# Performance work log

Hardware: AMD Instinct MI355X
Metric: run time of the kernel (lower is better)

Reference implementation:

```python
import jax, jax.numpy as jnp
import numpy as np

# module hyperparams (from init_kwargs)
C, O, G, E, W, KS = 64, 64, 16, 128, 7, 2
AH, AS = 2, 2              # activate_height, activate_stride
D = C // G                 # kernel depth per group = 4
N = O // G                 # filters per group = 4
EPS = 1e-5                 # BatchNorm eps
LEAKY = 0.01               # LeakyReLU negative slope
B, T = 2, 512


def setup_inputs() -> dict:
    key = jax.random.key(0)
    k1, k2 = jax.random.split(key)
    x = jax.random.normal(k1, (B, C, E, T), dtype=jnp.float32)
    weight = jax.random.normal(k2, (O, D, E, W), dtype=jnp.float32) * 0.05
    gamma = jnp.ones((O,), jnp.float32)
    beta = jnp.zeros((O,), jnp.float32)
    return {"x": x, "weight": weight, "gamma": gamma, "beta": beta}


def reference(x, weight, gamma, beta):
    b, c, f, T_in = x.shape
    pad = W // 2
    xp = jnp.pad(x, ((0, 0), (0, 0), (0, 0), (pad, pad)))
    t = (T_in + 2 * pad - W) // KS + 1
    # unfold: window index grid [t, W]
    idx = KS * jnp.arange(t)[:, None] + jnp.arange(W)[None, :]
    xu = xp[..., idx]                        # [b, c, f, t, W]
    xu = xu.reshape(b, G, D, f, t, W)        # channel = (g d), group-major
    wg = weight.reshape(G, N, D, f, W)       # out = (g n)
    # broadcast elementwise mul -> [b, g, n, d, f, t, w]
    y = xu[:, :, None] * wg[None, :, :, :, :, None, :]
    y = y.reshape(b, O, D, f, t, W)          # (g n) -> o
    # BatchNorm3d over channel O, training-mode batch stats (biased var)
    mean = y.mean(axis=(0, 2, 3, 4, 5), keepdims=True)
    var = y.var(axis=(0, 2, 3, 4, 5), keepdims=True)
    y = (y - mean) * jax.lax.rsqrt(var + EPS)
    bshape = (1, O, 1, 1, 1, 1)
    y = y * gamma.reshape(bshape) + beta.reshape(bshape)
    ys = y.sum(axis=(2, 5))                  # [b, o, f, t]
    yp = jax.lax.reduce_window(ys, jnp.float32(0), jax.lax.add,
                               (1, 1, AH, 1), (1, 1, AS, 1), 'VALID')  # [b,o,fo,t]
    return jnp.where(yp >= 0, yp, LEAKY * yp)
```

## Files before the change

kernel.cpp:

```cpp
#include <hip/hip_runtime.h>

constexpr int Cc = 64, Oc = 64, Gc = 16, Ec = 128, Wc = 7;
constexpr int Dc = 4, Nc = 4, Bc = 2, Tc = 512, TTc = 256, FOc = 64;
constexpr float EPSf = 1e-5f, LEAKYf = 0.01f;
constexpr float Minv = 1.0f / 1835008.0f;


__device__ __forceinline__ int FL4(int c) { return (c & 3) * 33 + (c >> 2); }

__global__ __launch_bounds__(256) void fused_k(const float* __restrict__ x,
                                               const float* __restrict__ wgt,
                                               float* __restrict__ raw,
                                               float* __restrict__ partials) {
  int bid = blockIdx.x;
  int fo2 = bid & 31;
  int g   = (bid >> 5) & 15;
  int b   = bid >> 9;
  int t   = threadIdx.x;

  __shared__ float xs[16 * 528];
  __shared__ float wsm[512];
  __shared__ float QS[16][2];
  __shared__ float QL[16][7];

  float4* xs4 = (float4*)xs;

#pragma unroll
  for (int k = 0; k < 8; ++k) {
    int idx = t + 256 * k;
    int lr = idx >> 7, jj = idx & 127;
    int fo_l = lr >> 3, dd = (lr >> 1) & 3, f2 = lr & 1;
    const float4* src = (const float4*)(
        x + ((size_t)((b * Cc + g * Dc + dd) * Ec + 4 * fo2 + 2 * fo_l + f2)) * Tc);
    float4 v = src[jj];
    xs4[lr * 132 + FL4(jj + 1)] = v;
  }
  if (t < 32) {
    int lr = t >> 1;
    int c = (t & 1) ? 129 : 0;
    xs4[lr * 132 + FL4(c)] = make_float4(0.f, 0.f, 0.f, 0.f);
  }
  if (t < 128) {
#pragma unroll
    for (int i = 0; i < 4; ++i) {
      int s = t * 4 + i;
      int w = s & 7, n = (s >> 3) & 3, lr8 = (s >> 5) & 7, fo_l = s >> 8;
      int o = g * Nc + n, dd = lr8 >> 1, f = 4 * fo2 + 2 * fo_l + (lr8 & 1);
      wsm[s] = (w < 7) ? wgt[((size_t)((o * Dc + dd) * Ec + f)) * Wc + w] : 0.f;
    }
  }
  __syncthreads();

  {
    int row = t >> 4, sub = t & 15;
    float se2 = 0.f, so2 = 0.f;
#pragma unroll
    for (int k = 0; k < 8; ++k) {
      int c = 1 + sub + 16 * k;
      float4 v = xs4[row * 132 + FL4(c)];
      se2 += v.x * v.x + v.z * v.z;
      so2 += v.y * v.y + v.w * v.w;
    }
#pragma unroll
    for (int off = 1; off < 16; off <<= 1) {
      se2 += __shfl_xor(se2, off);
      so2 += __shfl_xor(so2, off);
    }
    if (sub == 0) { QS[row][0] = se2; QS[row][1] = so2; }
  }

  int wv = t >> 6, j = t & 63;
  int fo_l = wv >> 1, n0 = (wv & 1) * 2;
  int fo = fo2 * 2 + fo_l;
  float acc0[4] = {0.f, 0.f, 0.f, 0.f}, acc1[4] = {0.f, 0.f, 0.f, 0.f};
#pragma unroll
  for (int lr8 = 0; lr8 < 8; ++lr8) {
    const float4* rb = xs4 + (fo_l * 8 + lr8) * 132;
    float4 X0 = rb[FL4(2 * j)];
    float4 X1 = rb[FL4(2 * j + 1)];
    float4 X2 = rb[FL4(2 * j + 2)];
    float4 X3 = rb[FL4(2 * j + 3)];
    float xq[16] = {X0.x, X0.y, X0.z, X0.w, X1.x, X1.y, X1.z, X1.w,
                    X2.x, X2.y, X2.z, X2.w, X3.x, X3.y, X3.z, X3.w};
    const float4* wb = (const float4*)&wsm[((fo_l * 8 + lr8) * 4 + n0) * 8];
    float4 Wa0 = wb[0], Wa1 = wb[1], Wb0 = wb[2], Wb1 = wb[3];
    float wA[7] = {Wa0.x, Wa0.y, Wa0.z, Wa0.w, Wa1.x, Wa1.y, Wa1.z};
    float wB[7] = {Wb0.x, Wb0.y, Wb0.z, Wb0.w, Wb1.x, Wb1.y, Wb1.z};
#pragma unroll
    for (int w = 0; w < 7; ++w) {
#pragma unroll
      for (int s = 0; s < 4; ++s) {
        float xv = xq[2 * s + w + 1];
        acc0[s] += xv * wA[w];
        acc1[s] += xv * wB[w];
      }
    }
  }
  {
    int o0 = g * Nc + n0;
    float4 r0 = make_float4(acc0[0], acc0[1], acc0[2], acc0[3]);
    float4 r1 = make_float4(acc1[0], acc1[1], acc1[2], acc1[3]);
    *(float4*)(raw + ((size_t)((b * Oc + o0) * FOc + fo)) * TTc + 4 * j) = r0;
    *(float4*)(raw + ((size_t)((b * Oc + o0 + 1) * FOc + fo)) * TTc + 4 * j) = r1;
  }
  {
    float ms0 = acc0[0] + acc0[1] + acc0[2] + acc0[3];
    float ms1 = acc1[0] + acc1[1] + acc1[2] + acc1[3];
#pragma unroll
    for (int off = 1; off < 64; off <<= 1) {
      ms0 += __shfl_xor(ms0, off);
      ms1 += __shfl_xor(ms1, off);
    }
    if (j == 0) {
      float* p = &partials[((size_t)((b * Gc + g) * FOc + fo)) * 8];
      p[n0] = ms0;
      p[n0 + 1] = ms1;
    }
  }
  __syncthreads();

  if (t < 16) {
    int row = t;
    const float* rowf = &xs[row * 528];
    float e509 = rowf[129], e510 = rowf[130], e511 = rowf[131];
    float e0 = rowf[132], e1 = rowf[133];
    float se2 = QS[row][0], so2 = QS[row][1];
    QL[row][0] = so2 - e509 * e509 - e511 * e511;
    QL[row][1] = se2 - e510 * e510;
    QL[row][2] = so2 - e511 * e511;
    QL[row][3] = se2;
    QL[row][4] = so2;
    QL[row][5] = se2 - e0 * e0;
    QL[row][6] = so2 - e1 * e1;
  }
  __syncthreads();
  if (t < 8) {
    int fl = t >> 2, n = t & 3;
    float vp = 0.f;
#pragma unroll
    for (int lr8 = 0; lr8 < 8; ++lr8) {
#pragma unroll
      for (int w = 0; w < 7; ++w) {
        float wt = wsm[((fl * 8 + lr8) * 4 + n) * 8 + w];
        vp += QL[fl * 8 + lr8][w] * wt * wt;
      }
    }
    partials[((size_t)((b * Gc + g) * FOc + fo2 * 2 + fl)) * 8 + 4 + n] = vp;
  }
}

__global__ __launch_bounds__(256) void finish_k(const float* __restrict__ raw,
                                                const float* __restrict__ partials,
                                                const float* __restrict__ gamma,
                                                const float* __restrict__ beta,
                                                float* __restrict__ out) {
  int bid = blockIdx.x;
  int seg = bid & 15;
  int o   = (bid >> 4) & 63;
  int b   = bid >> 10;
  int tid = threadIdx.x;
  int g = o >> 2, n = o & 3;

  __shared__ float red[2][2];
  __shared__ float sAC[2];

  float mp = 0.f, vp = 0.f;
  if (tid < 128) {
    int b2 = tid >> 6, fo = tid & 63;
    const float* p = &partials[(size_t)(((b2 << 4) | g) << 6 | fo) * 8];
    mp = p[n];
    vp = p[4 + n];
  }
#pragma unroll
  for (int off = 1; off < 64; off <<= 1) {
    mp += __shfl_xor(mp, off);
    vp += __shfl_xor(vp, off);
  }
  int lane = tid & 63, wv = tid >> 6;
  if (lane == 0 && wv < 2) { red[wv][0] = mp; red[wv][1] = vp; }
  __syncthreads();
  if (tid == 0) {
    float mean = (red[0][0] + red[1][0]) * Minv;
    float e2   = (red[0][1] + red[1][1]) * Minv;
    float var  = e2 - mean * mean;
    float a    = gamma[o] * rsqrtf(var + EPSf);
    sAC[0] = a;
    sAC[1] = 56.0f * (beta[o] - a * mean);
  }
  __syncthreads();

  float a = sAC[0], c = sAC[1];
  size_t base = ((size_t)(b * Oc + o)) * (FOc * TTc) + seg * 1024 + tid * 4;
  float4 v = *(const float4*)(raw + base);
  float4 res;
  float r0 = a * v.x + c; res.x = (r0 >= 0.f) ? r0 : LEAKYf * r0;
  float r1 = a * v.y + c; res.y = (r1 >= 0.f) ? r1 : LEAKYf * r1;
  float r2 = a * v.z + c; res.z = (r2 >= 0.f) ? r2 : LEAKYf * r2;
  float r3 = a * v.w + c; res.w = (r3 >= 0.f) ? r3 : LEAKYf * r3;
  *(float4*)(out + base) = res;
}

extern "C" void kernel_launch(void* const* d_in, const int* in_sizes, int n_in,
                              void* d_out, int out_size, void* d_ws, size_t ws_size,
                              hipStream_t stream) {
  (void)in_sizes; (void)n_in; (void)out_size; (void)ws_size;
  const float* x     = (const float*)d_in[0];
  const float* w     = (const float*)d_in[1];
  const float* gamma = (const float*)d_in[2];
  const float* beta  = (const float*)d_in[3];
  float* raw      = (float*)d_ws;
  float* partials = raw + (size_t)Bc * Oc * FOc * TTc;
  fused_k<<<dim3(Bc * Gc * 32), dim3(256), 0, stream>>>(x, w, raw, partials);
  finish_k<<<dim3(Bc * Oc * 16), dim3(256), 0, stream>>>(raw, partials, gamma,
                                                         beta, (float*)d_out);
}
```

Before: 91.89 us.

## Fuse conv and batchnorm finish via grid-wide atomic barrier, keeping results in registers

Result: slower. 135.3 us (+47.2%).

```diff
diff --git a/kernel.cpp b/kernel.cpp
--- a/kernel.cpp
+++ b/kernel.cpp
@@ -3,201 +3,226 @@
 constexpr int Cc = 64, Oc = 64, Gc = 16, Ec = 128, Wc = 7;
 constexpr int Dc = 4, Nc = 4, Bc = 2, Tc = 512, TTc = 256, FOc = 64;
 constexpr float EPSf = 1e-5f, LEAKYf = 0.01f;
+constexpr unsigned NBLK = 512;
 constexpr float Minv = 1.0f / 1835008.0f;
 
 
 __device__ __forceinline__ int FL4(int c) { return (c & 3) * 33 + (c >> 2); }
 
-__global__ __launch_bounds__(256) void fused_k(const float* __restrict__ x,
-                                               const float* __restrict__ wgt,
-                                               float* __restrict__ raw,
-                                               float* __restrict__ partials) {
+__global__ __launch_bounds__(256, 2) void coop_k(
+    const float* __restrict__ x, const float* __restrict__ wgt,
+    float* __restrict__ partials, unsigned* __restrict__ cnt,
+    const float* __restrict__ gamma, const float* __restrict__ beta,
+    float* __restrict__ out) {
   int bid = blockIdx.x;
-  int fo2 = bid & 31;
-  int g   = (bid >> 5) & 15;
-  int b   = bid >> 9;
-  int t   = threadIdx.x;
+  int fp = bid & 15;
+  int g  = (bid >> 4) & 15;
+  int b  = bid >> 8;
+  int t  = threadIdx.x;
 
   __shared__ float xs[16 * 528];
   __shared__ float wsm[512];
   __shared__ float QS[16][2];
   __shared__ float QL[16][7];
+  __shared__ float SR[2][8];
+  __shared__ float sA[4], sC[4];
 
   float4* xs4 = (float4*)xs;
-
-#pragma unroll
-  for (int k = 0; k < 8; ++k) {
-    int idx = t + 256 * k;
-    int lr = idx >> 7, jj = idx & 127;
-    int fo_l = lr >> 3, dd = (lr >> 1) & 3, f2 = lr & 1;
-    const float4* src = (const float4*)(
-        x + ((size_t)((b * Cc + g * Dc + dd) * Ec + 4 * fo2 + 2 * fo_l + f2)) * Tc);
-    float4 v = src[jj];
-    xs4[lr * 132 + FL4(jj + 1)] = v;
-  }
-  if (t < 32) {
-    int lr = t >> 1;
-    int c = (t & 1) ? 129 : 0;
-    xs4[lr * 132 + FL4(c)] = make_float4(0.f, 0.f, 0.f, 0.f);
-  }
-  if (t < 128) {
-#pragma unroll
-    for (int i = 0; i < 4; ++i) {
-      int s = t * 4 + i;
-      int w = s & 7, n = (s >> 3) & 3, lr8 = (s >> 5) & 7, fo_l = s >> 8;
-      int o = g * Nc + n, dd = lr8 >> 1, f = 4 * fo2 + 2 * fo_l + (lr8 & 1);
-      wsm[s] = (w < 7) ? wgt[((size_t)((o * Dc + dd) * Ec + f)) * Wc + w] : 0.f;
-    }
-  }
-  __syncthreads();
-
-  {
-    int row = t >> 4, sub = t & 15;
-    float se2 = 0.f, so2 = 0.f;
-#pragma unroll
-    for (int k = 0; k < 8; ++k) {
-      int c = 1 + sub + 16 * k;
-      float4 v = xs4[row * 132 + FL4(c)];
-      se2 += v.x * v.x + v.z * v.z;
-      so2 += v.y * v.y + v.w * v.w;
-    }
-#pragma unroll
-    for (int off = 1; off < 16; off <<= 1) {
-      se2 += __shfl_xor(se2, off);
-      so2 += __shfl_xor(so2, off);
-    }
-    if (sub == 0) { QS[row][0] = se2; QS[row][1] = so2; }
-  }
 
   int wv = t >> 6, j = t & 63;
   int fo_l = wv >> 1, n0 = (wv & 1) * 2;
-  int fo = fo2 * 2 + fo_l;
-  float acc0[4] = {0.f, 0.f, 0.f, 0.f}, acc1[4] = {0.f, 0.f, 0.f, 0.f};
-#pragma unroll
-  for (int lr8 = 0; lr8 < 8; ++lr8) {
-    const float4* rb = xs4 + (fo_l * 8 + lr8) * 132;
-    float4 X0 = rb[FL4(2 * j)];
-    float4 X1 = rb[FL4(2 * j + 1)];
-    float4 X2 = rb[FL4(2 * j + 2)];
-    float4 X3 = rb[FL4(2 * j + 3)];
-    float xq[16] = {X0.x, X0.y, X0.z, X0.w, X1.x, X1.y, X1.z, X1.w,
-                    X2.x, X2.y, X2.z, X2.w, X3.x, X3.y, X3.z, X3.w};
-    const float4* wb = (const float4*)&wsm[((fo_l * 8 + lr8) * 4 + n0) * 8];
-    float4 Wa0 = wb[0], Wa1 = wb[1], Wb0 = wb[2], Wb1 = wb[3];
-    float wA[7] = {Wa0.x, Wa0.y, Wa0.z, Wa0.w, Wa1.x, Wa1.y, Wa1.z};
-    float wB[7] = {Wb0.x, Wb0.y, Wb0.z, Wb0.w, Wb1.x, Wb1.y, Wb1.z};
-#pragma unroll
-    for (int w = 0; w < 7; ++w) {
-#pragma unroll
-      for (int s = 0; s < 4; ++s) {
-        float xv = xq[2 * s + w + 1];
-        acc0[s] += xv * wA[w];
-        acc1[s] += xv * wB[w];
-      }
-    }
-  }
+
+  float accT[2][2][4];
+
+#pragma unroll
+  for (int k = 0; k < 2; ++k) {
+    int fo2 = fp * 2 + k;
+
+#pragma unroll
+    for (int kk = 0; kk < 8; ++kk) {
+      int idx = t + 256 * kk;
+      int lr = idx >> 7, jj = idx & 127;
+      int flS = lr >> 3, dd = (lr >> 1) & 3, f2 = lr & 1;
+      const float4* src = (const float4*)(
+          x + ((size_t)((b * Cc + g * Dc + dd) * Ec + 4 * fo2 + 2 * flS + f2)) * Tc);
+      float4 v = src[jj];
+      xs4[lr * 132 + FL4(jj + 1)] = v;
+    }
+    if (t < 32) {
+      int lr = t >> 1;
+      int c = (t & 1) ? 129 : 0;
+      xs4[lr * 132 + FL4(c)] = make_float4(0.f, 0.f, 0.f, 0.f);
+    }
+    if (t < 128) {
+#pragma unroll
+      for (int i = 0; i < 4; ++i) {
+        int s = t * 4 + i;
+        int w = s & 7, n = (s >> 3) & 3, lr8 = (s >> 5) & 7, flS = s >> 8;
+        int o = g * Nc + n, dd = lr8 >> 1, f = 4 * fo2 + 2 * flS + (lr8 & 1);
+        wsm[s] = (w < 7) ? wgt[((size_t)((o * Dc + dd) * Ec + f)) * Wc + w] : 0.f;
+      }
+    }
+    __syncthreads();
+
+    {
+      int row = t >> 4, sub = t & 15;
+      float se2 = 0.f, so2 = 0.f;
+#pragma unroll
+      for (int kk = 0; kk < 8; ++kk) {
+        int c = 1 + sub + 16 * kk;
+        float4 v = xs4[row * 132 + FL4(c)];
+        se2 += v.x * v.x + v.z * v.z;
+        so2 += v.y * v.y + v.w * v.w;
+      }
+#pragma unroll
+      for (int off = 1; off < 16; off <<= 1) {
+        se2 += __shfl_xor(se2, off);
+        so2 += __shfl_xor(so2, off);
+      }
+      if (sub == 0) { QS[row][0] = se2; QS[row][1] = so2; }
+    }
+
+    float acc0[4] = {0.f, 0.f, 0.f, 0.f}, acc1[4] = {0.f, 0.f, 0.f, 0.f};
+#pragma unroll
+    for (int lr8 = 0; lr8 < 8; ++lr8) {
+      const float4* rb = xs4 + (fo_l * 8 + lr8) * 132;
+      float4 X0 = rb[FL4(2 * j)];
+      float4 X1 = rb[FL4(2 * j + 1)];
+      float4 X2 = rb[FL4(2 * j + 2)];
+      float4 X3 = rb[FL4(2 * j + 3)];
+      float xq[16] = {X0.x, X0.y, X0.z, X0.w, X1.x, X1.y, X1.z, X1.w,
+                      X2.x, X2.y, X2.z, X2.w, X3.x, X3.y, X3.z, X3.w};
+      const float4* wb = (const float4*)&wsm[((fo_l * 8 + lr8) * 4 + n0) * 8];
+      float4 Wa0 = wb[0], Wa1 = wb[1], Wb0 = wb[2], Wb1 = wb[3];
+      float wA[7] = {Wa0.x, Wa0.y, Wa0.z, Wa0.w, Wa1.x, Wa1.y, Wa1.z};
+      float wB[7] = {Wb0.x, Wb0.y, Wb0.z, Wb0.w, Wb1.x, Wb1.y, Wb1.z};
+#pragma unroll
+      for (int w = 0; w < 7; ++w) {
+#pragma unroll
+        for (int s = 0; s < 4; ++s) {
+          float xv = xq[2 * s + w + 1];
+          acc0[s] += xv * wA[w];
+          acc1[s] += xv * wB[w];
+        }
+      }
+    }
+#pragma unroll
+    for (int s = 0; s < 4; ++s) { accT[k][0][s] = acc0[s]; accT[k][1][s] = acc1[s]; }
+
+    {
+      float ms0 = acc0[0] + acc0[1] + acc0[2] + acc0[3];
+      float ms1 = acc1[0] + acc1[1] + acc1[2] + acc1[3];
+#pragma unroll
+      for (int off = 1; off < 64; off <<= 1) {
+        ms0 += __shfl_xor(ms0, off);
+        ms1 += __shfl_xor(ms1, off);
+      }
+      if (j == 0) {
+        int fo = fo2 * 2 + fo_l;
+        float* p = &partials[((size_t)((b * Gc + g) * FOc + fo)) * 8];
+        p[n0] = ms0;
+        p[n0 + 1] = ms1;
+      }
+    }
+    __syncthreads();
+
+    if (t < 16) {
+      int row = t;
+      const float* rowf = &xs[row * 528];
+      float e509 = rowf[129], e510 = rowf[130], e511 = rowf[131];
+      float e0 = rowf[132], e1 = rowf[133];
+      float se2 = QS[row][0], so2 = QS[row][1];
+      QL[row][0] = so2 - e509 * e509 - e511 * e511;
+      QL[row][1] = se2 - e510 * e510;
+      QL[row][2] = so2 - e511 * e511;
+      QL[row][3] = se2;
+      QL[row][4] = so2;
+      QL[row][5] = se2 - e0 * e0;
+      QL[row][6] = so2 - e1 * e1;
+    }
+    __syncthreads();
+    if (t < 8) {
+      int fl = t >> 2, n = t & 3;
+      float vp = 0.f;
+#pragma unroll
+      for (int lr8 = 0; lr8 < 8; ++lr8) {
+#pragma unroll
+        for (int w = 0; w < 7; ++w) {
+          float wt = wsm[((fl * 8 + lr8) * 4 + n) * 8 + w];
+          vp += QL[fl * 8 + lr8][w] * wt * wt;
+        }
+      }
+      partials[((size_t)((b * Gc + g) * FOc + fo2 * 2 + fl)) * 8 + 4 + n] = vp;
+    }
+    __syncthreads();
+  }
+
+  if (t == 0) {
+    __threadfence();
+    __hip_atomic_fetch_add(cnt, 1u, __ATOMIC_RELEASE, __HIP_MEMORY_SCOPE_AGENT);
+    while (__hip_atomic_load(cnt, __ATOMIC_ACQUIRE, __HIP_MEMORY_SCOPE_AGENT) <
+           NBLK) {
+      __builtin_amdgcn_s_sleep(4);
+    }
+    __threadfence();
+  }
+  __syncthreads();
+
   {
-    int o0 = g * Nc + n0;
-    float4 r0 = make_float4(acc0[0], acc0[1], acc0[2], acc0[3]);
-    float4 r1 = make_float4(acc1[0], acc1[1], acc1[2], acc1[3]);
-    *(float4*)(raw + ((size_t)((b * Oc + o0) * FOc + fo)) * TTc + 4 * j) = r0;
-    *(float4*)(raw + ((size_t)((b * Oc + o0 + 1) * FOc + fo)) * TTc + 4 * j) = r1;
-  }
-  {
-    float ms0 = acc0[0] + acc0[1] + acc0[2] + acc0[3];
-    float ms1 = acc1[0] + acc1[1] + acc1[2] + acc1[3];
+    float v0 = 0.f, v1 = 0.f, v2 = 0.f, v3 = 0.f;
+    float v4 = 0.f, v5 = 0.f, v6 = 0.f, v7 = 0.f;
+    if (t < 128) {
+      int b2 = t >> 6, fo = t & 63;
+      const float* p = &partials[((size_t)((b2 * Gc + g) * FOc + fo)) * 8];
+      float4 P0 = *(const float4*)p;
+      float4 P1 = *(const float4*)(p + 4);
+      v0 = P0.x; v1 = P0.y; v2 = P0.z; v3 = P0.w;
+      v4 = P1.x; v5 = P1.y; v6 = P1.z; v7 = P1.w;
+    }
 #pragma unroll
     for (int off = 1; off < 64; off <<= 1) {
-      ms0 += __shfl_xor(ms0, off);
-      ms1 += __shfl_xor(ms1, off);
-    }
-    if (j == 0) {
-      float* p = &partials[((size_t)((b * Gc + g) * FOc + fo)) * 8];
-      p[n0] = ms0;
-      p[n0 + 1] = ms1;
+      v0 += __shfl_xor(v0, off); v1 += __shfl_xor(v1, off);
+      v2 += __shfl_xor(v2, off); v3 += __shfl_xor(v3, off);
+      v4 += __shfl_xor(v4, off); v5 += __shfl_xor(v5, off);
+      v6 += __shfl_xor(v6, off); v7 += __shfl_xor(v7, off);
+    }
+    int lane = t & 63;
+    if (lane == 0 && wv < 2) {
+      SR[wv][0] = v0; SR[wv][1] = v1; SR[wv][2] = v2; SR[wv][3] = v3;
+      SR[wv][4] = v4; SR[wv][5] = v5; SR[wv][6] = v6; SR[wv][7] = v7;
     }
   }
   __syncthreads();
-
-  if (t < 16) {
-    int row = t;
-    const float* rowf = &xs[row * 528];
-    float e509 = rowf[129], e510 = rowf[130], e511 = rowf[131];
-    float e0 = rowf[132], e1 = rowf[133];
-    float se2 = QS[row][0], so2 = QS[row][1];
-    QL[row][0] = so2 - e509 * e509 - e511 * e511;
-    QL[row][1] = se2 - e510 * e510;
-    QL[row][2] = so2 - e511 * e511;
-    QL[row][3] = se2;
-    QL[row][4] = so2;
-    QL[row][5] = se2 - e0 * e0;
-    QL[row][6] = so2 - e1 * e1;
+  if (t < 4) {
+    float mean = (SR[0][t] + SR[1][t]) * Minv;
+    float e2   = (SR[0][4 + t] + SR[1][4 + t]) * Minv;
+    float var  = e2 - mean * mean;
+    int o = g * Nc + t;
+    float a = gamma[o] * rsqrtf(var + EPSf);
+    sA[t] = a;
+    sC[t] = 56.0f * (beta[o] - a * mean);
   }
   __syncthreads();
-  if (t < 8) {
-    int fl = t >> 2, n = t & 3;
-    float vp = 0.f;
-#pragma unroll
-    for (int lr8 = 0; lr8 < 8; ++lr8) {
-#pragma unroll
-      for (int w = 0; w < 7; ++w) {
-        float wt = wsm[((fl * 8 + lr8) * 4 + n) * 8 + w];
-        vp += QL[fl * 8 + lr8][w] * wt * wt;
-      }
-    }
-    partials[((size_t)((b * Gc + g) * FOc + fo2 * 2 + fl)) * 8 + 4 + n] = vp;
-  }
-}
-
-__global__ __launch_bounds__(256) void finish_k(const float* __restrict__ raw,
-                                                const float* __restrict__ partials,
-                                                const float* __restrict__ gamma,
-                                                const float* __restrict__ beta,
-                                                float* __restrict__ out) {
-  int bid = blockIdx.x;
-  int seg = bid & 15;
-  int o   = (bid >> 4) & 63;
-  int b   = bid >> 10;
-  int tid = threadIdx.x;
-  int g = o >> 2, n = o & 3;
-
-  __shared__ float red[2][2];
-  __shared__ float sAC[2];
-
-  float mp = 0.f, vp = 0.f;
-  if (tid < 128) {
-    int b2 = tid >> 6, fo = tid & 63;
-    const float* p = &partials[(size_t)(((b2 << 4) | g) << 6 | fo) * 8];
-    mp = p[n];
-    vp = p[4 + n];
-  }
-#pragma unroll
-  for (int off = 1; off < 64; off <<= 1) {
-    mp += __shfl_xor(mp, off);
-    vp += __shfl_xor(vp, off);
-  }
-  int lane = tid & 63, wv = tid >> 6;
-  if (lane == 0 && wv < 2) { red[wv][0] = mp; red[wv][1] = vp; }
-  __syncthreads();
-  if (tid == 0) {
-    float mean = (red[0][0] + red[1][0]) * Minv;
-    float e2   = (red[0][1] + red[1][1]) * Minv;
-    float var  = e2 - mean * mean;
-    float a    = gamma[o] * rsqrtf(var + EPSf);
-    sAC[0] = a;
-    sAC[1] = 56.0f * (beta[o] - a * mean);
-  }
-  __syncthreads();
-
-  float a = sAC[0], c = sAC[1];
-  size_t base = ((size_t)(b * Oc + o)) * (FOc * TTc) + seg * 1024 + tid * 4;
-  float4 v = *(const float4*)(raw + base);
-  float4 res;
-  float r0 = a * v.x + c; res.x = (r0 >= 0.f) ? r0 : LEAKYf * r0;
-  float r1 = a * v.y + c; res.y = (r1 >= 0.f) ? r1 : LEAKYf * r1;
-  float r2 = a * v.z + c; res.z = (r2 >= 0.f) ? r2 : LEAKYf * r2;
-  float r3 = a * v.w + c; res.w = (r3 >= 0.f) ? r3 : LEAKYf * r3;
-  *(float4*)(out + base) = res;
+
+  float a0 = sA[n0], c0 = sC[n0];
+  float a1 = sA[n0 + 1], c1 = sC[n0 + 1];
+  int o0 = g * Nc + n0;
+#pragma unroll
+  for (int k = 0; k < 2; ++k) {
+    int fo = (fp * 2 + k) * 2 + fo_l;
+    float4 r0, r1;
+    float u;
+    u = a0 * accT[k][0][0] + c0; r0.x = (u >= 0.f) ? u : LEAKYf * u;
+    u = a0 * accT[k][0][1] + c0; r0.y = (u >= 0.f) ? u : LEAKYf * u;
+    u = a0 * accT[k][0][2] + c0; r0.z = (u >= 0.f) ? u : LEAKYf * u;
+    u = a0 * accT[k][0][3] + c0; r0.w = (u >= 0.f) ? u : LEAKYf * u;
+    u = a1 * accT[k][1][0] + c1; r1.x = (u >= 0.f) ? u : LEAKYf * u;
+    u = a1 * accT[k][1][1] + c1; r1.y = (u >= 0.f) ? u : LEAKYf * u;
+    u = a1 * accT[k][1][2] + c1; r1.z = (u >= 0.f) ? u : LEAKYf * u;
+    u = a1 * accT[k][1][3] + c1; r1.w = (u >= 0.f) ? u : LEAKYf * u;
+    *(float4*)(out + ((size_t)((b * Oc + o0) * FOc + fo)) * TTc + 4 * j) = r0;
+    *(float4*)(out + ((size_t)((b * Oc + o0 + 1) * FOc + fo)) * TTc + 4 * j) = r1;
+  }
 }
 
 extern "C" void kernel_launch(void* const* d_in, const int* in_sizes, int n_in,
@@ -208,9 +233,9 @@
   const float* w     = (const float*)d_in[1];
   const float* gamma = (const float*)d_in[2];
   const float* beta  = (const float*)d_in[3];
-  float* raw      = (float*)d_ws;
-  float* partials = raw + (size_t)Bc * Oc * FOc * TTc;
-  fused_k<<<dim3(Bc * Gc * 32), dim3(256), 0, stream>>>(x, w, raw, partials);
-  finish_k<<<dim3(Bc * Oc * 16), dim3(256), 0, stream>>>(raw, partials, gamma,
-                                                         beta, (float*)d_out);
+  float* partials = (float*)d_ws;
+  unsigned* cnt = (unsigned*)((char*)d_ws + 2048 * 8 * sizeof(float));
+  hipMemsetAsync((void*)cnt, 0, sizeof(unsigned), stream);
+  coop_k<<<dim3(NBLK), dim3(256), 0, stream>>>(x, w, partials, cnt, gamma, beta,
+                                               (float*)d_out);
 }
```

## Compute BN stats analytically in a prepass and fuse normalize into conv

Applied to the files above, without the earlier changes.

Result: slower. 94.78 us (+3.1%).

```diff
diff --git a/kernel.cpp b/kernel.cpp
--- a/kernel.cpp
+++ b/kernel.cpp
@@ -6,12 +6,78 @@
 constexpr float Minv = 1.0f / 1835008.0f;
 
 
+__global__ __launch_bounds__(256) void stats_k(const float* __restrict__ x,
+                                               const float* __restrict__ wgt,
+                                               float* __restrict__ sums) {
+  int bid = blockIdx.x;
+  int ft = bid & 31;
+  int g  = (bid >> 5) & 15;
+  int b  = bid >> 9;
+  int t  = threadIdx.x;
+
+  __shared__ float RS[16][4];
+  __shared__ float ED[16][5];
+
+  int r = t >> 4, sub = t & 15;
+  int d = r >> 2, fi = r & 3;
+  const float4* src = (const float4*)(
+      x + ((size_t)((b * Cc + g * Dc + d) * Ec + 4 * ft + fi)) * Tc);
+
+  float se = 0.f, so = 0.f, se2 = 0.f, so2 = 0.f;
+#pragma unroll
+  for (int k = 0; k < 8; ++k) {
+    float4 v = src[sub + 16 * k];
+    se += v.x + v.z;  so += v.y + v.w;
+    se2 += v.x * v.x + v.z * v.z;
+    so2 += v.y * v.y + v.w * v.w;
+    if (k == 0 && sub == 0) { ED[r][0] = v.x; ED[r][1] = v.y; }
+    if (k == 7 && sub == 15) { ED[r][2] = v.y; ED[r][3] = v.z; ED[r][4] = v.w; }
+  }
+#pragma unroll
+  for (int off = 1; off < 16; off <<= 1) {
+    se  += __shfl_xor(se, off);  so  += __shfl_xor(so, off);
+    se2 += __shfl_xor(se2, off); so2 += __shfl_xor(so2, off);
+  }
+  if (sub == 0) { RS[r][0] = se; RS[r][1] = so; RS[r][2] = se2; RS[r][3] = so2; }
+  __syncthreads();
+
+  float md = 0.f, vd = 0.f;
+  if (t < 64) {
+    int r2 = t >> 2, n = t & 3;
+    float Se = RS[r2][0], So = RS[r2][1], Se2 = RS[r2][2], So2 = RS[r2][3];
+    float e0 = ED[r2][0], e1 = ED[r2][1];
+    float e509 = ED[r2][2], e510 = ED[r2][3], e511 = ED[r2][4];
+    float S[7] = {So - e509 - e511, Se - e510, So - e511, Se, So,
+                  Se - e0, So - e1};
+    float Q[7] = {So2 - e509 * e509 - e511 * e511, Se2 - e510 * e510,
+                  So2 - e511 * e511, Se2, So2, Se2 - e0 * e0, So2 - e1 * e1};
+    int d2 = r2 >> 2, fi2 = r2 & 3;
+    int o = g * Nc + n;
+    const float* wp = wgt + ((size_t)((o * Dc + d2) * Ec + 4 * ft + fi2)) * Wc;
+#pragma unroll
+    for (int w = 0; w < 7; ++w) {
+      float wt = wp[w];
+      md += wt * S[w];
+      vd += wt * wt * Q[w];
+    }
+  }
+#pragma unroll
+  for (int off = 4; off < 64; off <<= 1) {
+    md += __shfl_xor(md, off);
+    vd += __shfl_xor(vd, off);
+  }
+  if (t < 4) {
+    atomicAdd(&sums[(g * Nc + t) * 2], md);
+    atomicAdd(&sums[(g * Nc + t) * 2 + 1], vd);
+  }
+}
+
 __device__ __forceinline__ int FL4(int c) { return (c & 3) * 33 + (c >> 2); }
 
-__global__ __launch_bounds__(256) void fused_k(const float* __restrict__ x,
-                                               const float* __restrict__ wgt,
-                                               float* __restrict__ raw,
-                                               float* __restrict__ partials) {
+__global__ __launch_bounds__(256, 4) void conv_k(
+    const float* __restrict__ x, const float* __restrict__ wgt,
+    const float* __restrict__ sums, const float* __restrict__ gamma,
+    const float* __restrict__ beta, float* __restrict__ out) {
   int bid = blockIdx.x;
   int fo2 = bid & 31;
   int g   = (bid >> 5) & 15;
@@ -20,18 +86,15 @@
 
   __shared__ float xs[16 * 528];
   __shared__ float wsm[512];
-  __shared__ float QS[16][2];
-  __shared__ float QL[16][7];
-
   float4* xs4 = (float4*)xs;
 
 #pragma unroll
-  for (int k = 0; k < 8; ++k) {
-    int idx = t + 256 * k;
+  for (int kk = 0; kk < 8; ++kk) {
+    int idx = t + 256 * kk;
     int lr = idx >> 7, jj = idx & 127;
-    int fo_l = lr >> 3, dd = (lr >> 1) & 3, f2 = lr & 1;
+    int flS = lr >> 3, dd = (lr >> 1) & 3, f2 = lr & 1;
     const float4* src = (const float4*)(
-        x + ((size_t)((b * Cc + g * Dc + dd) * Ec + 4 * fo2 + 2 * fo_l + f2)) * Tc);
+        x + ((size_t)((b * Cc + g * Dc + dd) * Ec + 4 * fo2 + 2 * flS + f2)) * Tc);
     float4 v = src[jj];
     xs4[lr * 132 + FL4(jj + 1)] = v;
   }
@@ -44,34 +107,15 @@
 #pragma unroll
     for (int i = 0; i < 4; ++i) {
       int s = t * 4 + i;
-      int w = s & 7, n = (s >> 3) & 3, lr8 = (s >> 5) & 7, fo_l = s >> 8;
-      int o = g * Nc + n, dd = lr8 >> 1, f = 4 * fo2 + 2 * fo_l + (lr8 & 1);
+      int w = s & 7, n = (s >> 3) & 3, lr8 = (s >> 5) & 7, flS = s >> 8;
+      int o = g * Nc + n, dd = lr8 >> 1, f = 4 * fo2 + 2 * flS + (lr8 & 1);
       wsm[s] = (w < 7) ? wgt[((size_t)((o * Dc + dd) * Ec + f)) * Wc + w] : 0.f;
     }
   }
   __syncthreads();
 
-  {
-    int row = t >> 4, sub = t & 15;
-    float se2 = 0.f, so2 = 0.f;
-#pragma unroll
-    for (int k = 0; k < 8; ++k) {
-      int c = 1 + sub + 16 * k;
-      float4 v = xs4[row * 132 + FL4(c)];
-      se2 += v.x * v.x + v.z * v.z;
-      so2 += v.y * v.y + v.w * v.w;
-    }
-#pragma unroll
-    for (int off = 1; off < 16; off <<= 1) {
-      se2 += __shfl_xor(se2, off);
-      so2 += __shfl_xor(so2, off);
-    }
-    if (sub == 0) { QS[row][0] = se2; QS[row][1] = so2; }
-  }
-
   int wv = t >> 6, j = t & 63;
   int fo_l = wv >> 1, n0 = (wv & 1) * 2;
-  int fo = fo2 * 2 + fo_l;
   float acc0[4] = {0.f, 0.f, 0.f, 0.f}, acc1[4] = {0.f, 0.f, 0.f, 0.f};
 #pragma unroll
   for (int lr8 = 0; lr8 < 8; ++lr8) {
@@ -96,108 +140,28 @@
       }
     }
   }
-  {
-    int o0 = g * Nc + n0;
-    float4 r0 = make_float4(acc0[0], acc0[1], acc0[2], acc0[3]);
-    float4 r1 = make_float4(acc1[0], acc1[1], acc1[2], acc1[3]);
-    *(float4*)(raw + ((size_t)((b * Oc + o0) * FOc + fo)) * TTc + 4 * j) = r0;
-    *(float4*)(raw + ((size_t)((b * Oc + o0 + 1) * FOc + fo)) * TTc + 4 * j) = r1;
-  }
-  {
-    float ms0 = acc0[0] + acc0[1] + acc0[2] + acc0[3];
-    float ms1 = acc1[0] + acc1[1] + acc1[2] + acc1[3];
-#pragma unroll
-    for (int off = 1; off < 64; off <<= 1) {
-      ms0 += __shfl_xor(ms0, off);
-      ms1 += __shfl_xor(ms1, off);
-    }
-    if (j == 0) {
-      float* p = &partials[((size_t)((b * Gc + g) * FOc + fo)) * 8];
-      p[n0] = ms0;
-      p[n0 + 1] = ms1;
-    }
-  }
-  __syncthreads();
 
-  if (t < 16) {
-    int row = t;
-    const float* rowf = &xs[row * 528];
-    float e509 = rowf[129], e510 = rowf[130], e511 = rowf[131];
-    float e0 = rowf[132], e1 = rowf[133];
-    float se2 = QS[row][0], so2 = QS[row][1];
-    QL[row][0] = so2 - e509 * e509 - e511 * e511;
-    QL[row][1] = se2 - e510 * e510;
-    QL[row][2] = so2 - e511 * e511;
-    QL[row][3] = se2;
-    QL[row][4] = so2;
-    QL[row][5] = se2 - e0 * e0;
-    QL[row][6] = so2 - e1 * e1;
-  }
-  __syncthreads();
-  if (t < 8) {
-    int fl = t >> 2, n = t & 3;
-    float vp = 0.f;
-#pragma unroll
-    for (int lr8 = 0; lr8 < 8; ++lr8) {
-#pragma unroll
-      for (int w = 0; w < 7; ++w) {
-        float wt = wsm[((fl * 8 + lr8) * 4 + n) * 8 + w];
-        vp += QL[fl * 8 + lr8][w] * wt * wt;
-      }
-    }
-    partials[((size_t)((b * Gc + g) * FOc + fo2 * 2 + fl)) * 8 + 4 + n] = vp;
-  }
-}
+  int o0 = g * Nc + n0;
+  float m0 = sums[2 * o0] * Minv, E0 = sums[2 * o0 + 1] * Minv;
+  float a0 = gamma[o0] * rsqrtf(E0 - m0 * m0 + EPSf);
+  float c0 = 56.0f * (beta[o0] - a0 * m0);
+  float m1 = sums[2 * o0 + 2] * Minv, E1 = sums[2 * o0 + 3] * Minv;
+  float a1 = gamma[o0 + 1] * rsqrtf(E1 - m1 * m1 + EPSf);
+  float c1 = 56.0f * (beta[o0 + 1] - a1 * m1);
 
-__global__ __launch_bounds__(256) void finish_k(const float* __restrict__ raw,
-                                                const float* __restrict__ partials,
-                                                const float* __restrict__ gamma,
-                                                const float* __restrict__ beta,
-                                                float* __restrict__ out) {
-  int bid = blockIdx.x;
-  int seg = bid & 15;
-  int o   = (bid >> 4) & 63;
-  int b   = bid >> 10;
-  int tid = threadIdx.x;
-  int g = o >> 2, n = o & 3;
-
-  __shared__ float red[2][2];
-  __shared__ float sAC[2];
-
-  float mp = 0.f, vp = 0.f;
-  if (tid < 128) {
-    int b2 = tid >> 6, fo = tid & 63;
-    const float* p = &partials[(size_t)(((b2 << 4) | g) << 6 | fo) * 8];
-    mp = p[n];
-    vp = p[4 + n];
-  }
-#pragma unroll
-  for (int off = 1; off < 64; off <<= 1) {
-    mp += __shfl_xor(mp, off);
-    vp += __shfl_xor(vp, off);
-  }
-  int lane = tid & 63, wv = tid >> 6;
-  if (lane == 0 && wv < 2) { red[wv][0] = mp; red[wv][1] = vp; }
-  __syncthreads();
-  if (tid == 0) {
-    float mean = (red[0][0] + red[1][0]) * Minv;
-    float e2   = (red[0][1] + red[1][1]) * Minv;
-    float var  = e2 - mean * mean;
-    float a    = gamma[o] * rsqrtf(var + EPSf);
-    sAC[0] = a;
-    sAC[1] = 56.0f * (beta[o] - a * mean);
-  }
-  __syncthreads();
-
-  float a = sAC[0], c = sAC[1];
-  size_t base = ((size_t)(b * Oc + o)) * (FOc * TTc) + seg * 1024 + tid * 4;
-  float4 v = *(const float4*)(raw + base);
-  float4 res;
-  float r0 = a * v.x + c; res.x = (r0 >= 0.f) ? r0 : LEAKYf * r0;
-  float r1 = a * v.y + c; res.y = (r1 >= 0.f) ? r1 : LEAKYf * r1;
-  float r2 = a * v.z + c; res.z = (r2 >= 0.f) ? r2 : LEAKYf * r2;
-  float r3 = a * v.w + c; res.w = (r3 >= 0.f) ? r3 : LEAKYf * r3;
-  *(float4*)(out + base) = res;
+  int fo = fo2 * 2 + fo_l;
+  float4 r0, r1;
+  float u;
+  u = a0 * acc0[0] + c0; r0.x = (u >= 0.f) ? u : LEAKYf * u;
+  u = a0 * acc0[1] + c0; r0.y = (u >= 0.f) ? u : LEAKYf * u;
+  u = a0 * acc0[2] + c0; r0.z = (u >= 0.f) ? u : LEAKYf * u;
+  u = a0 * acc0[3] + c0; r0.w = (u >= 0.f) ? u : LEAKYf * u;
+  u = a1 * acc1[0] + c1; r1.x = (u >= 0.f) ? u : LEAKYf * u;
+  u = a1 * acc1[1] + c1; r1.y = (u >= 0.f) ? u : LEAKYf * u;
+  u = a1 * acc1[2] + c1; r1.z = (u >= 0.f) ? u : LEAKYf * u;
+  u = a1 * acc1[3] + c1; r1.w = (u >= 0.f) ? u : LEAKYf * u;
+  *(float4*)(out + ((size_t)((b * Oc + o0) * FOc + fo)) * TTc + 4 * j) = r0;
+  *(float4*)(out + ((size_t)((b * Oc + o0 + 1) * FOc + fo)) * TTc + 4 * j) = r1;
 }
 
 extern "C" void kernel_launch(void* const* d_in, const int* in_sizes, int n_in,
@@ -208,9 +172,9 @@
   const float* w     = (const float*)d_in[1];
   const float* gamma = (const float*)d_in[2];
   const float* beta  = (const float*)d_in[3];
-  float* raw      = (float*)d_ws;
-  float* partials = raw + (size_t)Bc * Oc * FOc * TTc;
-  fused_k<<<dim3(Bc * Gc * 32), dim3(256), 0, stream>>>(x, w, raw, partials);
-  finish_k<<<dim3(Bc * Oc * 16), dim3(256), 0, stream>>>(raw, partials, gamma,
-                                                         beta, (float*)d_out);
+  float* sums = (float*)d_ws;
+  hipMemsetAsync((void*)sums, 0, Oc * 2 * sizeof(float), stream);
+  stats_k<<<dim3(Bc * Gc * 32), dim3(256), 0, stream>>>(x, w, sums);
+  conv_k<<<dim3(Bc * Gc * 32), dim3(256), 0, stream>>>(x, w, sums, gamma, beta,
+                                                       (float*)d_out);
 }
```
